# Optimization experiments

Measured on AMD Instinct MI355X. Metric: run time of the kernel, lower is better.

Reference implementation:

```python
import jax, jax.numpy as jnp
import numpy as np

DIM = 1024
HEADS = 16
DIM_HEAD = 64
INNER = HEADS * DIM_HEAD  # 1024
MLP = 4096


def setup_inputs() -> dict:
    key = jax.random.key(0)
    ks = jax.random.split(key, 10)
    s = lambda k, shape, fan: jax.random.normal(k, shape, jnp.float32) * (fan ** -0.5)
    return {
        "x": jax.random.normal(ks[0], (4, 2048, DIM), jnp.float32),
        "ln1_g": jnp.ones((DIM,), jnp.float32),
        "ln1_b": jnp.zeros((DIM,), jnp.float32),
        "w_qkv": s(ks[1], (DIM, 3 * INNER), DIM),
        "w_out": s(ks[2], (INNER, DIM), INNER),
        "b_out": jnp.zeros((DIM,), jnp.float32),
        "ln2_g": jnp.ones((DIM,), jnp.float32),
        "ln2_b": jnp.zeros((DIM,), jnp.float32),
        "w1": s(ks[3], (DIM, MLP), DIM),
        "b1": jnp.zeros((MLP,), jnp.float32),
        "w2": s(ks[4], (MLP, DIM), MLP),
        "b2": jnp.zeros((DIM,), jnp.float32),
    }


def layernorm(x, g, b, eps=1e-5):
    mu = jnp.mean(x, axis=-1, keepdims=True)
    var = jnp.mean(jnp.square(x - mu), axis=-1, keepdims=True)
    return (x - mu) * jax.lax.rsqrt(var + eps) * g + b


def reference(x, ln1_g, ln1_b, w_qkv, w_out, b_out, ln2_g, ln2_b, w1, b1, w2, b2):
    b, n, d = x.shape
    h, dh = HEADS, DIM_HEAD
    scale = dh ** -0.5

    # Attention sub-block (pre-LN)
    xn = layernorm(x, ln1_g, ln1_b)
    qkv = xn @ w_qkv                                   # [b, n, 3*inner]
    q, k, v = jnp.split(qkv, 3, axis=-1)
    to_heads = lambda t: t.reshape(b, n, h, dh).transpose(0, 2, 1, 3)  # [b,h,n,dh]
    q, k, v = to_heads(q), to_heads(k), to_heads(v)
    dots = jnp.einsum('bhqd,bhkd->bhqk', q, k) * scale  # [b,h,n,n]
    attn = jax.nn.softmax(dots, axis=-1)
    out = jnp.einsum('bhqk,bhkd->bhqd', attn, v)        # [b,h,n,dh]
    out = out.transpose(0, 2, 1, 3).reshape(b, n, h * dh)
    x = x + out @ w_out + b_out

    # MLP sub-block (pre-LN)
    xn = layernorm(x, ln2_g, ln2_b)
    hdn = jax.nn.gelu(xn @ w1 + b1, approximate=False)
    x = x + hdn @ w2 + b2
    return x
```

## Files before the change

### kernel.cpp

```cpp
#include <hip/hip_runtime.h>
#include <hip/hip_bf16.h>
#include <math.h>

#define DIM   1024
#define HEADS 16
#define DH    64
#define SEQ   2048
#define BATCH 4
#define ROWS  (BATCH * SEQ)
#define MLP   4096
#define QKV3  (3 * DIM)

typedef __bf16    bf16x8 __attribute__((ext_vector_type(8)));
typedef __bf16    bf16x4 __attribute__((ext_vector_type(4)));
typedef float     f32x4  __attribute__((ext_vector_type(4)));
typedef unsigned int u32x2 __attribute__((ext_vector_type(2)));

__device__ inline void store_out(float* p, float v)           { *p = v; }
__device__ inline void store_out(__hip_bfloat16* p, float v)  { *p = __float2bfloat16(v); }

#define GLP(p) ((const __attribute__((address_space(1))) void*)(p))
#define LDP(p) ((__attribute__((address_space(3))) void*)(p))

__device__ inline float fast_exp2(float x) {
#if __has_builtin(__builtin_amdgcn_exp2f)
    return __builtin_amdgcn_exp2f(x);
#else
    return __expf(x * 0.69314718056f);
#endif
}

__device__ inline float fast_rcp(float x) {
#if __has_builtin(__builtin_amdgcn_rcpf)
    return __builtin_amdgcn_rcpf(x);
#else
    return 1.f / x;
#endif
}

__global__ __launch_bounds__(256) void ln_kernel(
    const float* __restrict__ x,
    const float* __restrict__ g,
    const float* __restrict__ b,
    __hip_bfloat16* __restrict__ y)
{
    const int row = blockIdx.x;
    const int tid = threadIdx.x;
    __shared__ float red[256];

    const float* xr = x + (size_t)row * DIM;
    float vals[4];
    float s = 0.f;
#pragma unroll
    for (int i = 0; i < 4; ++i) {
        vals[i] = xr[tid + i * 256];
        s += vals[i];
    }
    red[tid] = s; __syncthreads();
    for (int t = 128; t > 0; t >>= 1) { if (tid < t) red[tid] += red[tid + t]; __syncthreads(); }
    const float mu = red[0] * (1.f / DIM);
    __syncthreads();

    float vs = 0.f;
#pragma unroll
    for (int i = 0; i < 4; ++i) { float d = vals[i] - mu; vs += d * d; }
    red[tid] = vs; __syncthreads();
    for (int t = 128; t > 0; t >>= 1) { if (tid < t) red[tid] += red[tid + t]; __syncthreads(); }
    const float rstd = rsqrtf(red[0] * (1.f / DIM) + 1e-5f);

#pragma unroll
    for (int i = 0; i < 4; ++i) {
        const int c = tid + i * 256;
        float o = (vals[i] - mu) * rstd * g[c] + b[c];
        y[(size_t)row * DIM + c] = __float2bfloat16(o);
    }
}

__global__ __launch_bounds__(256) void transpose_w_kernel(
    const float* __restrict__ B, __bf16* __restrict__ BT,
    int Nfull, int r0, int c0, int Ksub)
{
    const int kb = blockIdx.x, nb = blockIdx.y;
    __shared__ float T[32][33];
    const int t  = threadIdx.x;
    const int r  = t >> 3;
    const int cq = (t & 7) * 4;

    f32x4 v = *(const f32x4*)(B + (size_t)(r0 + kb * 32 + r) * Nfull + c0 + nb * 32 + cq);
    T[r][cq] = v[0]; T[r][cq + 1] = v[1]; T[r][cq + 2] = v[2]; T[r][cq + 3] = v[3];
    __syncthreads();

    bf16x4 o;
#pragma unroll
    for (int i = 0; i < 4; ++i) o[i] = (__bf16)T[cq + i][r];
    *(bf16x4*)(BT + (size_t)(nb * 32 + r) * Ksub + kb * 32 + cq) = o;
}

template <typename OutT>
__global__ __launch_bounds__(512, 4) void gemm_bt_kernel(
    const __bf16* __restrict__ A,
    const __bf16* __restrict__ BT,
    const float* __restrict__ bias,
    const float* __restrict__ res,
    OutT* __restrict__ C,
    int M, int N, int K, int do_gelu)
{
    __shared__ __align__(16) __bf16 As[3][256 * 32];
    __shared__ __align__(16) __bf16 Bs[3][128 * 32];

    const int tid  = threadIdx.x;
    const int lane = tid & 63;
    const int w    = tid >> 6;
    const int q    = lane >> 4;
    const int c    = lane & 15;
    const int mw   = (w >> 1) * 64;
    const int nw   = (w & 1) * 64;

    const int nwg = gridDim.x;
    const int cpx = nwg >> 3;
    const int swz = ((int)blockIdx.x & 7) * cpx + ((int)blockIdx.x >> 3);
    const int colTiles = N >> 7;
    const int rowTile  = (swz / colTiles) * 256;
    const int colTile  = (swz % colTiles) * 128;

    const int sRow = tid >> 2;
    const int sK   = (tid & 3) * 8;
    const __bf16* Ap0 = A  + (size_t)(rowTile + sRow) * K + sK;
    const __bf16* Ap1 = A  + (size_t)(rowTile + 128 + sRow) * K + sK;
    const __bf16* Bp  = BT + (size_t)(colTile + sRow) * K + sK;
    const int wd = w * 512;

    f32x4 acc[4][4];
#pragma unroll
    for (int i = 0; i < 4; ++i)
#pragma unroll
        for (int j = 0; j < 4; ++j) acc[i][j] = (f32x4){0.f, 0.f, 0.f, 0.f};

    const int nt = K >> 5;

    __builtin_amdgcn_global_load_lds(GLP(Ap0), LDP(&As[0][wd]),        16, 0, 0);
    __builtin_amdgcn_global_load_lds(GLP(Ap1), LDP(&As[0][4096 + wd]), 16, 0, 0);
    __builtin_amdgcn_global_load_lds(GLP(Bp ), LDP(&Bs[0][wd]),        16, 0, 0);
    __builtin_amdgcn_global_load_lds(GLP(Ap0 + 32), LDP(&As[1][wd]),        16, 0, 0);
    __builtin_amdgcn_global_load_lds(GLP(Ap1 + 32), LDP(&As[1][4096 + wd]), 16, 0, 0);
    __builtin_amdgcn_global_load_lds(GLP(Bp  + 32), LDP(&Bs[1][wd]),        16, 0, 0);

    for (int t = 0; t < nt; ++t) {
        const int cur = t % 3;

        asm volatile("s_waitcnt vmcnt(3)" ::: "memory");
        if (t + 1 == nt) asm volatile("s_waitcnt vmcnt(0)" ::: "memory");
        __builtin_amdgcn_s_barrier();
        __builtin_amdgcn_sched_barrier(0);

        if (t + 2 < nt) {
            const int nb = (t + 2) % 3;
            const int ko = (t + 2) * 32;
            __builtin_amdgcn_global_load_lds(GLP(Ap0 + ko), LDP(&As[nb][wd]),        16, 0, 0);
            __builtin_amdgcn_global_load_lds(GLP(Ap1 + ko), LDP(&As[nb][4096 + wd]), 16, 0, 0);
            __builtin_amdgcn_global_load_lds(GLP(Bp  + ko), LDP(&Bs[nb][wd]),        16, 0, 0);
        }

        bf16x8 af[4], bf[4];
#pragma unroll
        for (int mt = 0; mt < 4; ++mt)
            af[mt] = *(const bf16x8*)(&As[cur][(mw + mt * 16 + c) * 32 + q * 8]);
#pragma unroll
        for (int nt2 = 0; nt2 < 4; ++nt2)
            bf[nt2] = *(const bf16x8*)(&Bs[cur][(nw + nt2 * 16 + c) * 32 + q * 8]);

#pragma unroll
        for (int mt = 0; mt < 4; ++mt)
#pragma unroll
            for (int nt2 = 0; nt2 < 4; ++nt2)
                acc[mt][nt2] = __builtin_amdgcn_mfma_f32_16x16x32_bf16(af[mt], bf[nt2], acc[mt][nt2], 0, 0, 0);
    }

#pragma unroll
    for (int nt2 = 0; nt2 < 4; ++nt2) {
        const int col = colTile + nw + nt2 * 16 + c;
        const float bv = bias ? bias[col] : 0.f;
#pragma unroll
        for (int mt = 0; mt < 4; ++mt) {
#pragma unroll
            for (int r = 0; r < 4; ++r) {
                const int row = rowTile + mw + mt * 16 + q * 4 + r;
                float v = acc[mt][nt2][r] + bv;
                if (do_gelu) {
                    const float y2 = fminf(1.5957691216057308f * v * (1.f + 0.044715f * v * v), 80.f);
                    const float e  = __expf(y2);
                    v = v * e * fast_rcp(e + 1.f);
                }
                if (res) v += res[(size_t)row * N + col];
                store_out(&C[(size_t)row * N + col], v);
            }
        }
    }
}

#define KB  64
#define QB  256
#define KTP 72
#define VTP 72
#define NT  (SEQ / KB)
#define NEG_M0_LOG2E  (-11.541560327111707f)
#define QSCALE_LOG2E  (0.18033688011112043f)

__global__ __launch_bounds__(256, 2) void flash_attn_kernel(
    const __hip_bfloat16* __restrict__ qkv,
    __hip_bfloat16* __restrict__ out)
{
    const int tid  = threadIdx.x;
    const int w    = tid >> 6;
    const int lane = tid & 63;
    const int quad = lane >> 4;
    const int c    = lane & 15;

    const int h = blockIdx.y;
    const int b = blockIdx.z;
    const size_t base = (size_t)b * SEQ;
    const int qbase = blockIdx.x * QB + w * 64;

    __shared__ __align__(16) __bf16 Kt[KB * KTP];
    __shared__ __align__(16) __bf16 Vt[DH * VTP];

    const __bf16* qkvb = (const __bf16*)qkv;

    bf16x8 aq[4][2];
#pragma unroll
    for (int qg = 0; qg < 4; ++qg)
#pragma unroll
        for (int kk = 0; kk < 2; ++kk) {
            bf16x8 t = *(const bf16x8*)(qkvb + (base + qbase + qg * 16 + c) * QKV3
                                        + h * DH + kk * 32 + quad * 8);
#pragma unroll
            for (int j = 0; j < 8; ++j) aq[qg][kk][j] = (__bf16)(QSCALE_LOG2E * (float)t[j]);
        }

    bf16x8 onesv;
#pragma unroll
    for (int j = 0; j < 8; ++j) onesv[j] = (__bf16)1.0f;

    f32x4 o[4][4];
#pragma unroll
    for (int qg = 0; qg < 4; ++qg)
#pragma unroll
        for (int ch = 0; ch < 4; ++ch) o[qg][ch] = (f32x4){0.f, 0.f, 0.f, 0.f};
    f32x4 ol[4] = {{0,0,0,0},{0,0,0,0},{0,0,0,0},{0,0,0,0}};

    const int sR = tid >> 3;
    const int sD = (tid & 7) * 8;
    const __bf16* Kg = qkvb + (base + sR) * QKV3 + DIM + h * DH + sD;

    const int vm = tid & 7;
    const int d0 = (tid >> 3) * 2;
    const __bf16* Vg = qkvb + (base + 8 * vm) * QKV3 + 2 * DIM + h * DH + d0;
    const int bpos = 32 * (vm >> 2) + 16 * (vm & 1) + 4 * ((vm >> 1) & 1);

    bf16x8 kA, kB_;
    unsigned vv[8];
    kA  = *(const bf16x8*)(Kg);
    kB_ = *(const bf16x8*)(Kg + (size_t)32 * QKV3);
#pragma unroll
    for (int j = 0; j < 8; ++j)
        vv[j] = *(const unsigned*)(Vg + (size_t)j * QKV3);

    for (int kt = 0; kt < NT; ++kt) {
        *(bf16x8*)(&Kt[sR * KTP + sD])        = kA;
        *(bf16x8*)(&Kt[(sR + 32) * KTP + sD]) = kB_;
        {
            const unsigned lo01 = (vv[0] & 0xFFFFu) | (vv[1] << 16);
            const unsigned lo23 = (vv[2] & 0xFFFFu) | (vv[3] << 16);
            const unsigned lo45 = (vv[4] & 0xFFFFu) | (vv[5] << 16);
            const unsigned lo67 = (vv[6] & 0xFFFFu) | (vv[7] << 16);
            const unsigned hi01 = (vv[0] >> 16) | (vv[1] & 0xFFFF0000u);
            const unsigned hi23 = (vv[2] >> 16) | (vv[3] & 0xFFFF0000u);
            const unsigned hi45 = (vv[4] >> 16) | (vv[5] & 0xFFFF0000u);
            const unsigned hi67 = (vv[6] >> 16) | (vv[7] & 0xFFFF0000u);
            *(u32x2*)(&Vt[(d0    ) * VTP + bpos])     = (u32x2){lo01, lo23};
            *(u32x2*)(&Vt[(d0    ) * VTP + bpos + 8]) = (u32x2){lo45, lo67};
            *(u32x2*)(&Vt[(d0 + 1) * VTP + bpos])     = (u32x2){hi01, hi23};
            *(u32x2*)(&Vt[(d0 + 1) * VTP + bpos + 8]) = (u32x2){hi45, hi67};
        }
        __syncthreads();

        if (kt + 1 < NT) {
            const size_t koff = (size_t)(kt + 1) * KB * QKV3;
            kA  = *(const bf16x8*)(Kg + koff);
            kB_ = *(const bf16x8*)(Kg + koff + (size_t)32 * QKV3);
#pragma unroll
            for (int j = 0; j < 8; ++j)
                vv[j] = *(const unsigned*)(Vg + koff + (size_t)j * QKV3);
        }

        bf16x8 kf[4][2];
#pragma unroll
        for (int kg = 0; kg < 4; ++kg)
#pragma unroll
            for (int kk = 0; kk < 2; ++kk)
                kf[kg][kk] = *(const bf16x8*)(&Kt[(kg * 16 + c) * KTP + kk * 32 + quad * 8]);

        bf16x8 ap[4][2];
#pragma unroll
        for (int qg = 0; qg < 4; ++qg) {
            f32x4 st[4];
#pragma unroll
            for (int kg = 0; kg < 4; ++kg)
                st[kg] = (f32x4){NEG_M0_LOG2E, NEG_M0_LOG2E, NEG_M0_LOG2E, NEG_M0_LOG2E};
            __builtin_amdgcn_s_setprio(1);
#pragma unroll
            for (int kg = 0; kg < 4; ++kg)
#pragma unroll
                for (int kk = 0; kk < 2; ++kk)
                    st[kg] = __builtin_amdgcn_mfma_f32_16x16x32_bf16(kf[kg][kk], aq[qg][kk], st[kg], 0, 0, 0);
            __builtin_amdgcn_s_setprio(0);

#pragma unroll
            for (int kg = 0; kg < 4; ++kg)
#pragma unroll
                for (int r = 0; r < 4; ++r)
                    ap[qg][kg >> 1][(kg & 1) * 4 + r] = (__bf16)fast_exp2(st[kg][r]);
        }

        __builtin_amdgcn_s_setprio(1);
#pragma unroll
        for (int qg = 0; qg < 4; ++qg) {
            ol[qg] = __builtin_amdgcn_mfma_f32_16x16x32_bf16(ap[qg][0], onesv, ol[qg], 0, 0, 0);
            ol[qg] = __builtin_amdgcn_mfma_f32_16x16x32_bf16(ap[qg][1], onesv, ol[qg], 0, 0, 0);
        }
#pragma unroll
        for (int h2 = 0; h2 < 2; ++h2)
#pragma unroll
            for (int ch = 0; ch < 4; ++ch) {
                bf16x8 bv = *(const bf16x8*)(&Vt[(ch * 16 + c) * VTP + h2 * 32 + quad * 8]);
#pragma unroll
                for (int qg = 0; qg < 4; ++qg)
                    o[qg][ch] = __builtin_amdgcn_mfma_f32_16x16x32_bf16(ap[qg][h2], bv, o[qg][ch], 0, 0, 0);
            }
        __builtin_amdgcn_s_setprio(0);
        __syncthreads();
    }

#pragma unroll
    for (int qg = 0; qg < 4; ++qg) {
#pragma unroll
        for (int r = 0; r < 4; ++r) {
            const float inv = 1.f / ol[qg][r];
            const size_t row = base + qbase + qg * 16 + quad * 4 + r;
#pragma unroll
            for (int ch = 0; ch < 4; ++ch)
                out[row * DIM + h * DH + ch * 16 + c] = __float2bfloat16(o[qg][ch][r] * inv);
        }
    }
}

extern "C" void kernel_launch(void* const* d_in, const int* in_sizes, int n_in,
                              void* d_out, int out_size, void* d_ws, size_t ws_size,
                              hipStream_t stream)
{
    const float* x     = (const float*)d_in[0];
    const float* ln1_g = (const float*)d_in[1];
    const float* ln1_b = (const float*)d_in[2];
    const float* w_qkv = (const float*)d_in[3];
    const float* w_out = (const float*)d_in[4];
    const float* b_out = (const float*)d_in[5];
    const float* ln2_g = (const float*)d_in[6];
    const float* ln2_b = (const float*)d_in[7];
    const float* w1    = (const float*)d_in[8];
    const float* b1    = (const float*)d_in[9];
    const float* w2    = (const float*)d_in[10];
    const float* b2    = (const float*)d_in[11];
    float* out = (float*)d_out;

    char* ws = (char*)d_ws;
    const size_t MiB = 1024 * 1024;
    __hip_bfloat16* X   = (__hip_bfloat16*)(ws);
    __bf16*         wT  = (__bf16*)(ws + 16 * MiB);
    __hip_bfloat16* qkv = (__hip_bfloat16*)(ws + 24 * MiB);
    __bf16*         hdn = (__bf16*)(ws + 24 * MiB);

    dim3 blk(256);
    dim3 blk512(512);

    transpose_w_kernel<<<dim3(DIM / 32, QKV3 / 32), blk, 0, stream>>>(w_qkv, wT, QKV3, 0, 0, DIM);
    ln_kernel<<<dim3(ROWS), blk, 0, stream>>>(x, ln1_g, ln1_b, X);
    gemm_bt_kernel<__hip_bfloat16><<<dim3((QKV3 / 128) * (ROWS / 256)), blk512, 0, stream>>>(
        (const __bf16*)X, wT, nullptr, nullptr, qkv, ROWS, QKV3, DIM, 0);
    flash_attn_kernel<<<dim3(SEQ / QB, HEADS, BATCH), blk, 0, stream>>>(qkv, X);
    transpose_w_kernel<<<dim3(DIM / 32, DIM / 32), blk, 0, stream>>>(w_out, wT, DIM, 0, 0, DIM);
    gemm_bt_kernel<float><<<dim3((DIM / 128) * (ROWS / 256)), blk512, 0, stream>>>(
        (const __bf16*)X, wT, b_out, x, out, ROWS, DIM, DIM, 0);
    ln_kernel<<<dim3(ROWS), blk, 0, stream>>>(out, ln2_g, ln2_b, X);

    transpose_w_kernel<<<dim3(DIM / 32, 2048 / 32), blk, 0, stream>>>(w1, wT, MLP, 0, 0, DIM);
    gemm_bt_kernel<__hip_bfloat16><<<dim3((2048 / 128) * (ROWS / 256)), blk512, 0, stream>>>(
        (const __bf16*)X, wT, b1, nullptr, (__hip_bfloat16*)hdn, ROWS, 2048, DIM, 1);
    transpose_w_kernel<<<dim3(2048 / 32, DIM / 32), blk, 0, stream>>>(w2, wT, DIM, 0, 0, 2048);
    gemm_bt_kernel<float><<<dim3((DIM / 128) * (ROWS / 256)), blk512, 0, stream>>>(
        hdn, wT, b2, out, out, ROWS, DIM, 2048, 0);

    transpose_w_kernel<<<dim3(DIM / 32, 2048 / 32), blk, 0, stream>>>(w1, wT, MLP, 0, 2048, DIM);
    gemm_bt_kernel<__hip_bfloat16><<<dim3((2048 / 128) * (ROWS / 256)), blk512, 0, stream>>>(
        (const __bf16*)X, wT, b1 + 2048, nullptr, (__hip_bfloat16*)hdn, ROWS, 2048, DIM, 1);
    transpose_w_kernel<<<dim3(2048 / 32, DIM / 32), blk, 0, stream>>>(w2, wT, DIM, 2048, 0, 2048);
    gemm_bt_kernel<float><<<dim3((DIM / 128) * (ROWS / 256)), blk512, 0, stream>>>(
        hdn, wT, nullptr, out, out, ROWS, DIM, 2048, 0);
}
```

Before: 603.4 us.

## Template GEMM on tile width, use 256x256 tiles and double buffering

Makes the GEMM tile width a template parameter and runs the QKV and MLP-up GEMMs with 256x256 tiles, each wave owning a 128x64 sub-tile, to raise operand reuse and cut global and LDS traffic per FLOP. The triple-buffered pipeline with explicit vmcnt waits is replaced by a simpler two-stage buffer with a __syncthreads per K step. Tile assignment is also changed to walk row tiles first. The cost is more accumulator registers per wave, fewer workgroups for the wide GEMMs, and less latency hiding from the shallower pipeline and extra barriers.

```diff
diff --git a/kernel.cpp b/kernel.cpp
--- a/kernel.cpp
+++ b/kernel.cpp
@@ -96,7 +96,7 @@
     *(bf16x4*)(BT + (size_t)(nb * 32 + r) * Ksub + kb * 32 + cq) = o;
 }
 
-template <typename OutT>
+template <typename OutT, int BN>
 __global__ __launch_bounds__(512, 4) void gemm_bt_kernel(
     const __bf16* __restrict__ A,
     const __bf16* __restrict__ BT,
@@ -105,75 +105,78 @@
     OutT* __restrict__ C,
     int M, int N, int K, int do_gelu)
 {
-    __shared__ __align__(16) __bf16 As[3][256 * 32];
-    __shared__ __align__(16) __bf16 Bs[3][128 * 32];
+    constexpr int WC  = (BN == 256) ? 4 : 2;
+    constexpr int MT  = (BN == 256) ? 8 : 4;
+    constexpr int WTM = 16 * MT;
+
+    __shared__ __align__(16) __bf16 As[2][256 * 32];
+    __shared__ __align__(16) __bf16 Bs[2][BN * 32];
 
     const int tid  = threadIdx.x;
     const int lane = tid & 63;
     const int w    = tid >> 6;
     const int q    = lane >> 4;
     const int c    = lane & 15;
-    const int mw   = (w >> 1) * 64;
-    const int nw   = (w & 1) * 64;
+    const int mw   = (w / WC) * WTM;
+    const int nw   = (w % WC) * 64;
 
     const int nwg = gridDim.x;
     const int cpx = nwg >> 3;
     const int swz = ((int)blockIdx.x & 7) * cpx + ((int)blockIdx.x >> 3);
-    const int colTiles = N >> 7;
-    const int rowTile  = (swz / colTiles) * 256;
-    const int colTile  = (swz % colTiles) * 128;
+    const int rowTiles = M >> 8;
+    const int rowTile  = (swz % rowTiles) * 256;
+    const int colTile  = (swz / rowTiles) * BN;
 
     const int sRow = tid >> 2;
     const int sK   = (tid & 3) * 8;
     const __bf16* Ap0 = A  + (size_t)(rowTile + sRow) * K + sK;
     const __bf16* Ap1 = A  + (size_t)(rowTile + 128 + sRow) * K + sK;
-    const __bf16* Bp  = BT + (size_t)(colTile + sRow) * K + sK;
-    const int wd = w * 512;
-
-    f32x4 acc[4][4];
-#pragma unroll
-    for (int i = 0; i < 4; ++i)
+    const __bf16* Bp0 = BT + (size_t)(colTile + sRow) * K + sK;
+    const __bf16* Bp1 = BT + (size_t)(colTile + 128 + sRow) * K + sK;
+    const int td8 = tid * 8;
+
+    f32x4 acc[MT][4];
+#pragma unroll
+    for (int i = 0; i < MT; ++i)
 #pragma unroll
         for (int j = 0; j < 4; ++j) acc[i][j] = (f32x4){0.f, 0.f, 0.f, 0.f};
 
     const int nt = K >> 5;
 
-    __builtin_amdgcn_global_load_lds(GLP(Ap0), LDP(&As[0][wd]),        16, 0, 0);
-    __builtin_amdgcn_global_load_lds(GLP(Ap1), LDP(&As[0][4096 + wd]), 16, 0, 0);
-    __builtin_amdgcn_global_load_lds(GLP(Bp ), LDP(&Bs[0][wd]),        16, 0, 0);
-    __builtin_amdgcn_global_load_lds(GLP(Ap0 + 32), LDP(&As[1][wd]),        16, 0, 0);
-    __builtin_amdgcn_global_load_lds(GLP(Ap1 + 32), LDP(&As[1][4096 + wd]), 16, 0, 0);
-    __builtin_amdgcn_global_load_lds(GLP(Bp  + 32), LDP(&Bs[1][wd]),        16, 0, 0);
+    __builtin_amdgcn_global_load_lds(GLP(Ap0), LDP(&As[0][td8]),        16, 0, 0);
+    __builtin_amdgcn_global_load_lds(GLP(Ap1), LDP(&As[0][4096 + td8]), 16, 0, 0);
+    __builtin_amdgcn_global_load_lds(GLP(Bp0), LDP(&Bs[0][td8]),        16, 0, 0);
+    if (BN == 256)
+        __builtin_amdgcn_global_load_lds(GLP(Bp1), LDP(&Bs[0][4096 + td8]), 16, 0, 0);
+    __syncthreads();
 
     for (int t = 0; t < nt; ++t) {
-        const int cur = t % 3;
-
-        asm volatile("s_waitcnt vmcnt(3)" ::: "memory");
-        if (t + 1 == nt) asm volatile("s_waitcnt vmcnt(0)" ::: "memory");
-        __builtin_amdgcn_s_barrier();
-        __builtin_amdgcn_sched_barrier(0);
-
-        if (t + 2 < nt) {
-            const int nb = (t + 2) % 3;
-            const int ko = (t + 2) * 32;
-            __builtin_amdgcn_global_load_lds(GLP(Ap0 + ko), LDP(&As[nb][wd]),        16, 0, 0);
-            __builtin_amdgcn_global_load_lds(GLP(Ap1 + ko), LDP(&As[nb][4096 + wd]), 16, 0, 0);
-            __builtin_amdgcn_global_load_lds(GLP(Bp  + ko), LDP(&Bs[nb][wd]),        16, 0, 0);
-        }
-
-        bf16x8 af[4], bf[4];
-#pragma unroll
-        for (int mt = 0; mt < 4; ++mt)
+        const int cur = t & 1;
+        if (t + 1 < nt) {
+            const int nb = cur ^ 1;
+            const int ko = (t + 1) * 32;
+            __builtin_amdgcn_global_load_lds(GLP(Ap0 + ko), LDP(&As[nb][td8]),        16, 0, 0);
+            __builtin_amdgcn_global_load_lds(GLP(Ap1 + ko), LDP(&As[nb][4096 + td8]), 16, 0, 0);
+            __builtin_amdgcn_global_load_lds(GLP(Bp0 + ko), LDP(&Bs[nb][td8]),        16, 0, 0);
+            if (BN == 256)
+                __builtin_amdgcn_global_load_lds(GLP(Bp1 + ko), LDP(&Bs[nb][4096 + td8]), 16, 0, 0);
+        }
+
+        bf16x8 af[MT], bf[4];
+#pragma unroll
+        for (int mt = 0; mt < MT; ++mt)
             af[mt] = *(const bf16x8*)(&As[cur][(mw + mt * 16 + c) * 32 + q * 8]);
 #pragma unroll
         for (int nt2 = 0; nt2 < 4; ++nt2)
             bf[nt2] = *(const bf16x8*)(&Bs[cur][(nw + nt2 * 16 + c) * 32 + q * 8]);
 
 #pragma unroll
-        for (int mt = 0; mt < 4; ++mt)
+        for (int mt = 0; mt < MT; ++mt)
 #pragma unroll
             for (int nt2 = 0; nt2 < 4; ++nt2)
                 acc[mt][nt2] = __builtin_amdgcn_mfma_f32_16x16x32_bf16(af[mt], bf[nt2], acc[mt][nt2], 0, 0, 0);
+
+        __syncthreads();
     }
 
 #pragma unroll
@@ -181,7 +184,7 @@
         const int col = colTile + nw + nt2 * 16 + c;
         const float bv = bias ? bias[col] : 0.f;
 #pragma unroll
-        for (int mt = 0; mt < 4; ++mt) {
+        for (int mt = 0; mt < MT; ++mt) {
 #pragma unroll
             for (int r = 0; r < 4; ++r) {
                 const int row = rowTile + mw + mt * 16 + q * 4 + r;
@@ -384,25 +387,25 @@
 
     transpose_w_kernel<<<dim3(DIM / 32, QKV3 / 32), blk, 0, stream>>>(w_qkv, wT, QKV3, 0, 0, DIM);
     ln_kernel<<<dim3(ROWS), blk, 0, stream>>>(x, ln1_g, ln1_b, X);
-    gemm_bt_kernel<__hip_bfloat16><<<dim3((QKV3 / 128) * (ROWS / 256)), blk512, 0, stream>>>(
+    gemm_bt_kernel<__hip_bfloat16, 256><<<dim3((QKV3 / 256) * (ROWS / 256)), blk512, 0, stream>>>(
         (const __bf16*)X, wT, nullptr, nullptr, qkv, ROWS, QKV3, DIM, 0);
     flash_attn_kernel<<<dim3(SEQ / QB, HEADS, BATCH), blk, 0, stream>>>(qkv, X);
     transpose_w_kernel<<<dim3(DIM / 32, DIM / 32), blk, 0, stream>>>(w_out, wT, DIM, 0, 0, DIM);
-    gemm_bt_kernel<float><<<dim3((DIM / 128) * (ROWS / 256)), blk512, 0, stream>>>(
+    gemm_bt_kernel<float, 128><<<dim3((DIM / 128) * (ROWS / 256)), blk512, 0, stream>>>(
         (const __bf16*)X, wT, b_out, x, out, ROWS, DIM, DIM, 0);
     ln_kernel<<<dim3(ROWS), blk, 0, stream>>>(out, ln2_g, ln2_b, X);
 
     transpose_w_kernel<<<dim3(DIM / 32, 2048 / 32), blk, 0, stream>>>(w1, wT, MLP, 0, 0, DIM);
-    gemm_bt_kernel<__hip_bfloat16><<<dim3((2048 / 128) * (ROWS / 256)), blk512, 0, stream>>>(
+    gemm_bt_kernel<__hip_bfloat16, 256><<<dim3((2048 / 256) * (ROWS / 256)), blk512, 0, stream>>>(
         (const __bf16*)X, wT, b1, nullptr, (__hip_bfloat16*)hdn, ROWS, 2048, DIM, 1);
     transpose_w_kernel<<<dim3(2048 / 32, DIM / 32), blk, 0, stream>>>(w2, wT, DIM, 0, 0, 2048);
-    gemm_bt_kernel<float><<<dim3((DIM / 128) * (ROWS / 256)), blk512, 0, stream>>>(
+    gemm_bt_kernel<float, 128><<<dim3((DIM / 128) * (ROWS / 256)), blk512, 0, stream>>>(
         hdn, wT, b2, out, out, ROWS, DIM, 2048, 0);
 
     transpose_w_kernel<<<dim3(DIM / 32, 2048 / 32), blk, 0, stream>>>(w1, wT, MLP, 0, 2048, DIM);
-    gemm_bt_kernel<__hip_bfloat16><<<dim3((2048 / 128) * (ROWS / 256)), blk512, 0, stream>>>(
+    gemm_bt_kernel<__hip_bfloat16, 256><<<dim3((2048 / 256) * (ROWS / 256)), blk512, 0, stream>>>(
         (const __bf16*)X, wT, b1 + 2048, nullptr, (__hip_bfloat16*)hdn, ROWS, 2048, DIM, 1);
     transpose_w_kernel<<<dim3(2048 / 32, DIM / 32), blk, 0, stream>>>(w2, wT, DIM, 2048, 0, 2048);
-    gemm_bt_kernel<float><<<dim3((DIM / 128) * (ROWS / 256)), blk512, 0, stream>>>(
+    gemm_bt_kernel<float, 128><<<dim3((DIM / 128) * (ROWS / 256)), blk512, 0, stream>>>(
         hdn, wT, nullptr, out, out, ROWS, DIM, 2048, 0);
 }
```

Measured after the change: 1.297 ms. +114.9%, slower.
